# Kernel tuning notes

Hardware: AMD Instinct MI355X
Metric: run time of the kernel (lower is better)

Reference implementation:

```python
import jax, jax.numpy as jnp
import numpy as np

B, S, E = 8, 4096, 128

def _prelu(x, a):
    return jnp.where(x >= 0, x, a * x)

def setup_inputs() -> dict:
    key = jax.random.key(0)
    ks = jax.random.split(key, 7)
    lim = 1.0 / np.sqrt(E)
    x = jax.random.normal(ks[0], (B, S, E), dtype=jnp.float32)
    Wq = jax.random.uniform(ks[1], (E, E), jnp.float32, -lim, lim)
    Wk = jax.random.uniform(ks[2], (E, E), jnp.float32, -lim, lim)
    Wv = jax.random.uniform(ks[3], (E, E), jnp.float32, -lim, lim)
    bq = jax.random.uniform(ks[4], (E,), jnp.float32, -lim, lim)
    bk = jax.random.uniform(ks[5], (E,), jnp.float32, -lim, lim)
    bv = jax.random.uniform(ks[6], (E,), jnp.float32, -lim, lim)
    # PReLU default: single shared slope initialized to 0.25
    aq = jnp.array(0.25, dtype=jnp.float32)
    ak = jnp.array(0.25, dtype=jnp.float32)
    av = jnp.array(0.25, dtype=jnp.float32)
    return {"x": x, "Wq": Wq, "bq": bq, "aq": aq,
            "Wk": Wk, "bk": bk, "ak": ak,
            "Wv": Wv, "bv": bv, "av": av}

def reference(x, Wq, bq, aq, Wk, bk, ak, Wv, bv, av):
    # Linear (y = x @ W.T + b) followed by PReLU, per nn.Sequential(Linear, PReLU)
    qx = _prelu(jnp.einsum('bse,fe->bsf', x, Wq) + bq, aq)  # [B,S,E]
    kx = _prelu(jnp.einsum('bse,fe->bsf', x, Wk) + bk, ak)
    vx = _prelu(jnp.einsum('bse,fe->bsf', x, Wv) + bv, av)
    scale = 1.0 / jnp.sqrt(jnp.asarray(E, dtype=x.dtype))
    qk = jnp.einsum('bqe,bke->bqk', qx, kx) * scale  # [B,S,S]
    attn = jax.nn.softmax(qk, axis=2)
    return jnp.einsum('bqk,bke->bqe', attn, vx)  # [B,S,E]
```

## Files before the change

### kernel.cpp

```cpp
#include <hip/hip_runtime.h>
#include <hip/hip_bf16.h>
#include <stdint.h>

typedef __bf16 bf16x8 __attribute__((ext_vector_type(8)));
typedef float f32x4 __attribute__((ext_vector_type(4)));
typedef float f32x16 __attribute__((ext_vector_type(16)));
typedef unsigned int u32x4 __attribute__((ext_vector_type(4)));

static constexpr int Bn = 8, Sn = 4096, En = 128;

__device__ __forceinline__ unsigned short f2bf(float f) {
  unsigned u = __builtin_bit_cast(unsigned, f);
  u += 0x7fffu + ((u >> 16) & 1u);
  return (unsigned short)(u >> 16);
}

__device__ __forceinline__ unsigned cvtpk(float a, float b) {
  unsigned r;
  asm("v_cvt_pk_bf16_f32 %0, %1, %2" : "=v"(r) : "v"(a), "v"(b));
  return r;
}

__device__ __forceinline__ void plswap(unsigned &a, unsigned &b) {
  asm("v_permlane32_swap_b32 %0, %1" : "+v"(a), "+v"(b));
}

__global__ __launch_bounds__(256) void qkv_kernel(
    const float* __restrict__ x,
    const float* __restrict__ Wq, const float* __restrict__ bq, const float* __restrict__ aq,
    const float* __restrict__ Wk, const float* __restrict__ bk, const float* __restrict__ ak,
    const float* __restrict__ Wv, const float* __restrict__ bv, const float* __restrict__ av,
    unsigned short* __restrict__ qo, unsigned short* __restrict__ ko,
    unsigned short* __restrict__ vto)
{
  __shared__ __align__(16) unsigned short xs[64 * 136];
  __shared__ __align__(16) unsigned short wsh[128 * 136];
  const int tid = threadIdx.x;
  const int r0 = blockIdx.x * 64;

  for (int i = 0; i < 8; ++i) {
    int cid = tid + i * 256;
    int row = cid >> 5, c4 = cid & 31;
    const float4 v = *(const float4*)&x[(size_t)(r0 + row) * 128 + c4 * 4];
    unsigned short* d = &xs[row * 136 + c4 * 4];
    d[0] = f2bf(v.x); d[1] = f2bf(v.y); d[2] = f2bf(v.z); d[3] = f2bf(v.w);
  }

  const int lane = tid & 63, wid = tid >> 6;
  const int g = lane >> 4, ln = lane & 15;
  const float* Ws[3] = {Wq, Wk, Wv};
  const float* Bs[3] = {bq, bk, bv};
  const float* As[3] = {aq, ak, av};
  bf16x8 afrag[4];

  for (int mat = 0; mat < 3; ++mat) {
    __syncthreads();
    for (int i = 0; i < 16; ++i) {
      int cid = tid + i * 256;
      int row = cid >> 5, c4 = cid & 31;
      const float4 v = *(const float4*)&Ws[mat][row * 128 + c4 * 4];
      unsigned short* d = &wsh[row * 136 + c4 * 4];
      d[0] = f2bf(v.x); d[1] = f2bf(v.y); d[2] = f2bf(v.z); d[3] = f2bf(v.w);
    }
    __syncthreads();

    if (mat == 0) {
      for (int ks = 0; ks < 4; ++ks)
        afrag[ks] = *(const bf16x8*)&xs[(wid * 16 + ln) * 136 + ks * 32 + g * 8];
    }
    const float alpha = As[mat][0];
    f32x4 acc[8];
    for (int nt = 0; nt < 8; ++nt) acc[nt] = (f32x4)(0.f);
    for (int nt = 0; nt < 8; ++nt)
      for (int ks = 0; ks < 4; ++ks) {
        bf16x8 bfrag = *(const bf16x8*)&wsh[(nt * 16 + ln) * 136 + ks * 32 + g * 8];
        acc[nt] = __builtin_amdgcn_mfma_f32_16x16x32_bf16(afrag[ks], bfrag, acc[nt], 0, 0, 0);
      }
    const int mbase = r0 + wid * 16 + g * 4;
    for (int nt = 0; nt < 8; ++nt) {
      const int n = nt * 16 + ln;
      const float bias = Bs[mat][n];
      float vv[4];
      for (int r = 0; r < 4; ++r) {
        float t = acc[nt][r] + bias;
        vv[r] = t >= 0.f ? t : alpha * t;
      }
      if (mat == 0) {
        for (int r = 0; r < 4; ++r) qo[(size_t)(mbase + r) * 128 + n] = f2bf(vv[r]);
      } else if (mat == 1) {
        for (int r = 0; r < 4; ++r) ko[(size_t)(mbase + r) * 128 + n] = f2bf(vv[r]);
      } else {
        const int b = mbase >> 12, s = mbase & 4095;
        ushort4 pk;
        pk.x = f2bf(vv[0]); pk.y = f2bf(vv[1]); pk.z = f2bf(vv[2]); pk.w = f2bf(vv[3]);
        *(ushort4*)&vto[(size_t)b * (En * Sn) + (size_t)n * Sn + s] = pk;
      }
    }
  }
}

__device__ __forceinline__ void load_tiles(const char* kg, const char* vg, int key0,
                                           int tid, uint4* kreg, uint4* vreg) {
  const char* ksrc = kg + (size_t)key0 * 256;
  #pragma unroll
  for (int i = 0; i < 2; ++i) kreg[i] = *(const uint4*)(ksrc + (tid + i * 512) * 16);
  #pragma unroll
  for (int i = 0; i < 2; ++i) {
    int o = (tid + i * 512) * 16;
    vreg[i] = *(const uint4*)(vg + (size_t)(o >> 7) * 8192 + (size_t)key0 * 2 + (o & 127));
  }
}

__device__ __forceinline__ void store_tiles(char* kd, char* vd, int tid,
                                            const uint4* kreg, const uint4* vreg) {
  #pragma unroll
  for (int i = 0; i < 2; ++i) {
    int o = (tid + i * 512) * 16;
    *(uint4*)(kd + (o ^ (((o >> 8) & 7) << 4))) = kreg[i];
  }
  #pragma unroll
  for (int i = 0; i < 2; ++i) {
    int o = (tid + i * 512) * 16;
    *(uint4*)(vd + (o ^ (((o >> 7) & 7) << 4))) = vreg[i];
  }
}

template <int KSPLIT>
__global__ __launch_bounds__(512, 2) void attn_kernel(
    const unsigned short* __restrict__ q,
    const unsigned short* __restrict__ k,
    const unsigned short* __restrict__ vt,
    float* __restrict__ opart, float* __restrict__ mpart,
    float* __restrict__ lpart, float* __restrict__ out)
{
  __shared__ __align__(16) char smem[65536];
  const int tid = threadIdx.x;
  const int lane = tid & 63, wid = tid >> 6;
  const int NS = 8 * KSPLIT;
  const int bid = blockIdx.x;
  const int s_ = bid % NS;
  const int qt = bid / NS;
  const int b  = s_ / KSPLIT;
  const int kh = s_ % KSPLIT;
  const int hi = lane >> 5, ln = lane & 31;
  const size_t bOff = (size_t)b * Sn * En;
  const char* kg = (const char*)(k + bOff);
  const char* vg = (const char*)(vt + (size_t)b * En * Sn);

  const int qrow = qt * 256 + wid * 32 + ln;
  bf16x8 qf[8];
  #pragma unroll
  for (int s = 0; s < 8; ++s)
    qf[s] = *(const bf16x8*)((const char*)(q + bOff) + (size_t)qrow * 256 + s * 32 + hi * 16);

  f32x16 acc[4];
  #pragma unroll
  for (int et = 0; et < 4; ++et) acc[et] = (f32x16)(0.f);
  float m_run = -1e30f, lsum = 0.f;

  const int nkt = (Sn / KSPLIT) / 64;
  const int kbase = kh * (Sn / KSPLIT);
  const float cst = 1.4426950408889634f * 0.08838834764831845f;

  auto compute = [&](const char* kl, const char* vl) {
    f32x16 st0 = (f32x16)(0.f), st1 = (f32x16)(0.f);
    __builtin_amdgcn_s_setprio(1);
    #pragma unroll
    for (int s = 0; s < 8; ++s) {
      const int cb = (32 * s + 16 * hi) ^ ((ln & 7) << 4);
      bf16x8 kf0 = *(const bf16x8*)(kl + ln * 256 + cb);
      bf16x8 kf1 = *(const bf16x8*)(kl + (32 + ln) * 256 + cb);
      st0 = __builtin_amdgcn_mfma_f32_32x32x16_bf16(kf0, qf[s], st0, 0, 0, 0);
      st1 = __builtin_amdgcn_mfma_f32_32x32x16_bf16(kf1, qf[s], st1, 0, 0, 0);
    }
    __builtin_amdgcn_s_setprio(0);

    float t16[16];
    #pragma unroll
    for (int i = 0; i < 16; ++i) t16[i] = fmaxf(st0[i], st1[i]);
    float t8[8];
    #pragma unroll
    for (int i = 0; i < 8; ++i) t8[i] = fmaxf(t16[i], t16[i + 8]);
    float t4[4];
    #pragma unroll
    for (int i = 0; i < 4; ++i) t4[i] = fmaxf(t8[i], t8[i + 4]);
    float vtile = fmaxf(fmaxf(t4[0], t4[1]), fmaxf(t4[2], t4[3])) * cst;
    vtile = fmaxf(vtile, __shfl_xor(vtile, 32));

    if (__any(vtile > m_run + 8.0f)) {
      float mnew = fmaxf(m_run, vtile);
      float al = __builtin_amdgcn_exp2f(m_run - mnew);
      #pragma unroll
      for (int et = 0; et < 4; ++et) acc[et] *= al;
      lsum *= al;
      m_run = mnew;
    }

    float p[32];
    #pragma unroll
    for (int i = 0; i < 16; ++i) p[i]      = __builtin_amdgcn_exp2f(fmaf(st0[i], cst, -m_run));
    #pragma unroll
    for (int i = 0; i < 16; ++i) p[16 + i] = __builtin_amdgcn_exp2f(fmaf(st1[i], cst, -m_run));

    float s16[16];
    #pragma unroll
    for (int i = 0; i < 16; ++i) s16[i] = p[i] + p[16 + i];
    float s8[8];
    #pragma unroll
    for (int i = 0; i < 8; ++i) s8[i] = s16[i] + s16[i + 8];
    float s4[4];
    #pragma unroll
    for (int i = 0; i < 4; ++i) s4[i] = s8[i] + s8[i + 4];
    float tsum = (s4[0] + s4[1]) + (s4[2] + s4[3]);
    tsum += __shfl_xor(tsum, 32);
    lsum += tsum;

    unsigned wa[8], wb[8];
    #pragma unroll
    for (int g2 = 0; g2 < 8; ++g2) {
      wa[g2] = cvtpk(p[4 * g2], p[4 * g2 + 1]);
      wb[g2] = cvtpk(p[4 * g2 + 2], p[4 * g2 + 3]);
    }
    bf16x8 pb[4];
    #pragma unroll
    for (int ks = 0; ks < 4; ++ks) {
      unsigned w0 = wa[2 * ks], w2 = wa[2 * ks + 1];
      plswap(w0, w2);
      unsigned w1 = wb[2 * ks], w3 = wb[2 * ks + 1];
      plswap(w1, w3);
      u32x4 w = {w0, w1, w2, w3};
      pb[ks] = __builtin_bit_cast(bf16x8, w);
    }

    __builtin_amdgcn_s_setprio(1);
    #pragma unroll
    for (int ks = 0; ks < 4; ++ks) {
      const int cb = (32 * ks + 16 * hi) ^ ((ln & 7) << 4);
      #pragma unroll
      for (int et = 0; et < 4; ++et) {
        bf16x8 vf = *(const bf16x8*)(vl + (32 * et + ln) * 128 + cb);
        acc[et] = __builtin_amdgcn_mfma_f32_32x32x16_bf16(vf, pb[ks], acc[et], 0, 0, 0);
      }
    }
    __builtin_amdgcn_s_setprio(0);
  };

  uint4 kregA[2], vregA[2], kregB[2], vregB[2];
  load_tiles(kg, vg, kbase, tid, kregA, vregA);
  store_tiles(smem, smem + 32768, tid, kregA, vregA);
  if (nkt > 1) load_tiles(kg, vg, kbase + 64, tid, kregA, vregA);
  __syncthreads();

  for (int kt = 0; kt < nkt; kt += 2) {
    if (kt + 2 < nkt) load_tiles(kg, vg, kbase + (kt + 2) * 64, tid, kregB, vregB);
    compute(smem, smem + 32768);
    __syncthreads();
    if (kt + 1 < nkt)
      store_tiles(smem + 16384, smem + 32768 + 16384, tid, kregA, vregA);
    __syncthreads();
    if (kt + 3 < nkt) load_tiles(kg, vg, kbase + (kt + 3) * 64, tid, kregA, vregA);
    if (kt + 1 < nkt)
      compute(smem + 16384, smem + 32768 + 16384);
    __syncthreads();
    if (kt + 2 < nkt)
      store_tiles(smem, smem + 32768, tid, kregB, vregB);
    __syncthreads();
  }

  if (KSPLIT > 1 && lane < 32) {
    const size_t idx = (size_t)kh * (Bn * Sn) + (size_t)b * Sn + qt * 256 + wid * 32 + ln;
    mpart[idx] = m_run;
    lpart[idx] = lsum;
  }

  __syncthreads();
  const float inv = (KSPLIT == 1) ? (1.0f / lsum) : 1.0f;
  char* sl = smem + wid * 8192;
  char* outb;
  if (KSPLIT == 1)
    outb = (char*)(out + ((size_t)b * Sn + qt * 256 + wid * 32) * En);
  else
    outb = (char*)(opart + ((size_t)kh * (Bn * Sn) + (size_t)b * Sn + qt * 256 + wid * 32) * En);

  #pragma unroll
  for (int h = 0; h < 2; ++h) {
    #pragma unroll
    for (int e2 = 0; e2 < 2; ++e2) {
      const int et = 2 * h + e2;
      #pragma unroll
      for (int rg = 0; rg < 4; ++rg) {
        f32x4 v;
        #pragma unroll
        for (int j = 0; j < 4; ++j) v[j] = acc[et][rg * 4 + j] * inv;
        const int addr = ln * 256 + e2 * 128 + rg * 32 + hi * 16;
        *(f32x4*)(sl + (addr ^ ((ln & 7) << 4))) = v;
      }
    }
    asm volatile("s_waitcnt lgkmcnt(0)" ::: "memory");
    __builtin_amdgcn_sched_barrier(0);
    #pragma unroll
    for (int i = 0; i < 8; ++i) {
      const int flat = i * 1024 + lane * 16;
      const int qr = flat >> 8, col = flat & 255;
      f32x4 v = *(const f32x4*)(sl + ((qr * 256 + col) ^ ((qr & 7) << 4)));
      *(f32x4*)(outb + (size_t)qr * 512 + h * 256 + col) = v;
    }
    if (h == 0) {
      asm volatile("s_waitcnt lgkmcnt(0)" ::: "memory");
      __builtin_amdgcn_sched_barrier(0);
    }
  }
}

template <int NSPLIT>
__global__ __launch_bounds__(256) void combine_kernel(
    const float* __restrict__ op, const float* __restrict__ mp,
    const float* __restrict__ lp, float* __restrict__ out)
{
  const int idx = blockIdx.x * 256 + threadIdx.x;
  const int row = idx >> 5;
  const int BS = Bn * Sn;
  const size_t NO = (size_t)BS * En / 4;
  float m = -1e30f;
  #pragma unroll
  for (int j = 0; j < NSPLIT; ++j) m = fmaxf(m, mp[j * BS + row]);
  float den = 0.f;
  f32x4 sum = (f32x4)(0.f);
  #pragma unroll
  for (int j = 0; j < NSPLIT; ++j) {
    const float w = __builtin_amdgcn_exp2f(mp[j * BS + row] - m);
    den += w * lp[j * BS + row];
    f32x4 o = ((const f32x4*)op)[j * NO + idx];
    sum += o * w;
  }
  const float inv = 1.f / den;
  ((f32x4*)out)[idx] = sum * inv;
}

extern "C" void kernel_launch(void* const* d_in, const int* in_sizes, int n_in,
                              void* d_out, int out_size, void* d_ws, size_t ws_size,
                              hipStream_t stream) {
  const float* x  = (const float*)d_in[0];
  const float* Wq = (const float*)d_in[1];
  const float* bq = (const float*)d_in[2];
  const float* aq = (const float*)d_in[3];
  const float* Wk = (const float*)d_in[4];
  const float* bk = (const float*)d_in[5];
  const float* ak = (const float*)d_in[6];
  const float* Wv = (const float*)d_in[7];
  const float* bv = (const float*)d_in[8];
  const float* av = (const float*)d_in[9];

  const size_t BSE = (size_t)Bn * Sn * En;
  const size_t BS  = (size_t)Bn * Sn;
  char* base = (char*)d_ws;
  unsigned short* qws = (unsigned short*)base;
  unsigned short* kws = qws + BSE;
  unsigned short* vws = kws + BSE;
  const size_t fixed = 3 * BSE * 2;
  float* opart = (float*)(base + fixed);

  auto need = [&](int j) { return fixed + (size_t)j * BSE * 4 + (size_t)j * BS * 8; };
  int split = 1;
  if (ws_size >= need(2)) split = 2;

  float* mpart = (float*)(base + fixed + (size_t)split * BSE * 4);
  float* lpart = mpart + (size_t)split * BS;

  qkv_kernel<<<512, 256, 0, stream>>>(x, Wq, bq, aq, Wk, bk, ak, Wv, bv, av,
                                      qws, kws, vws);
  if (split == 2) {
    attn_kernel<2><<<256, 512, 0, stream>>>(qws, kws, vws, opart, mpart, lpart,
                                            (float*)d_out);
    combine_kernel<2><<<4096, 256, 0, stream>>>(opart, mpart, lpart, (float*)d_out);
  } else {
    attn_kernel<1><<<128, 512, 0, stream>>>(qws, kws, vws, opart, mpart, lpart,
                                            (float*)d_out);
  }
}
```

Before: 154.6 us.

## Software-pipeline QK^T of next tile with softmax and PV of current tile

```diff
diff --git a/kernel.cpp b/kernel.cpp
--- a/kernel.cpp
+++ b/kernel.cpp
@@ -162,8 +162,8 @@
   const int kbase = kh * (Sn / KSPLIT);
   const float cst = 1.4426950408889634f * 0.08838834764831845f;
 
-  auto compute = [&](const char* kl, const char* vl) {
-    f32x16 st0 = (f32x16)(0.f), st1 = (f32x16)(0.f);
+  auto qk = [&](const char* kl, f32x16& st0, f32x16& st1) {
+    st0 = (f32x16)(0.f); st1 = (f32x16)(0.f);
     __builtin_amdgcn_s_setprio(1);
     #pragma unroll
     for (int s = 0; s < 8; ++s) {
@@ -174,7 +174,9 @@
       st1 = __builtin_amdgcn_mfma_f32_32x32x16_bf16(kf1, qf[s], st1, 0, 0, 0);
     }
     __builtin_amdgcn_s_setprio(0);
-
+  };
+
+  auto sm_pv = [&](const char* vl, const f32x16& st0, const f32x16& st1) {
     float t16[16];
     #pragma unroll
     for (int i = 0; i < 16; ++i) t16[i] = fmaxf(st0[i], st1[i]);
@@ -245,27 +247,41 @@
     __builtin_amdgcn_s_setprio(0);
   };
 
-  uint4 kregA[2], vregA[2], kregB[2], vregB[2];
-  load_tiles(kg, vg, kbase, tid, kregA, vregA);
-  store_tiles(smem, smem + 32768, tid, kregA, vregA);
-  if (nkt > 1) load_tiles(kg, vg, kbase + 64, tid, kregA, vregA);
+  char* const k0 = smem;
+  char* const k1 = smem + 16384;
+  char* const v0 = smem + 32768;
+  char* const v1 = smem + 32768 + 16384;
+
+  uint4 kreg[2], vreg[2];
+  load_tiles(kg, vg, kbase, tid, kreg, vreg);
+  store_tiles(k0, v0, tid, kreg, vreg);
+  load_tiles(kg, vg, kbase + 64, tid, kreg, vreg);
   __syncthreads();
-
-  for (int kt = 0; kt < nkt; kt += 2) {
-    if (kt + 2 < nkt) load_tiles(kg, vg, kbase + (kt + 2) * 64, tid, kregB, vregB);
-    compute(smem, smem + 32768);
-    __syncthreads();
-    if (kt + 1 < nkt)
-      store_tiles(smem + 16384, smem + 32768 + 16384, tid, kregA, vregA);
-    __syncthreads();
-    if (kt + 3 < nkt) load_tiles(kg, vg, kbase + (kt + 3) * 64, tid, kregA, vregA);
-    if (kt + 1 < nkt)
-      compute(smem + 16384, smem + 32768 + 16384);
-    __syncthreads();
-    if (kt + 2 < nkt)
-      store_tiles(smem, smem + 32768, tid, kregB, vregB);
-    __syncthreads();
-  }
+  f32x16 sA0, sA1, sB0, sB1;
+  qk(k0, sA0, sA1);
+
+  int kt = 0;
+  for (; kt + 2 < nkt; kt += 2) {
+    __syncthreads();
+    store_tiles(k1, v1, tid, kreg, vreg);
+    __syncthreads();
+    load_tiles(kg, vg, kbase + (kt + 2) * 64, tid, kreg, vreg);
+    qk(k1, sB0, sB1);
+    sm_pv(v0, sA0, sA1);
+
+    __syncthreads();
+    store_tiles(k0, v0, tid, kreg, vreg);
+    __syncthreads();
+    if (kt + 3 < nkt) load_tiles(kg, vg, kbase + (kt + 3) * 64, tid, kreg, vreg);
+    qk(k0, sA0, sA1);
+    sm_pv(v1, sB0, sB1);
+  }
+  __syncthreads();
+  store_tiles(k1, v1, tid, kreg, vreg);
+  __syncthreads();
+  qk(k1, sB0, sB1);
+  sm_pv(v0, sA0, sA1);
+  sm_pv(v1, sB0, sB1);
 
   if (KSPLIT > 1 && lane < 32) {
     const size_t idx = (size_t)kh * (Bn * Sn) + (size_t)b * Sn + qt * 256 + wid * 32 + ln;
```

New measurement: 152.4 us. No clear change (-1.4%).
